# Kernel tuning notes

Measured on AMD Instinct MI355X. Metric: run time of the kernel, lower is better.

## Reference

```python
import jax, jax.numpy as jnp
import numpy as np

N = 8192       # nodes per graph
E = 262144     # edges per graph (avg degree 32)
D_IN, D_H, D_OUT = 128, 256, 64


def _gcn_layer(x, src, dst, W, b, n):
    # PyG GCNConv: add self-loops, symmetric normalization D^-1/2 (A+I) D^-1/2, then + bias
    xw = x @ W
    loop = jnp.arange(n)
    src_f = jnp.concatenate([src, loop])
    dst_f = jnp.concatenate([dst, loop])
    deg = jax.ops.segment_sum(jnp.ones(src_f.shape[0], x.dtype), dst_f, num_segments=n)
    dinv = jax.lax.rsqrt(jnp.maximum(deg, jnp.asarray(1e-12, x.dtype)))
    norm = dinv[src_f] * dinv[dst_f]                      # [E+N]
    msg = xw[src_f] * norm[:, None]                       # gather + scale
    return jax.ops.segment_sum(msg, dst_f, num_segments=n) + b


def _cross_attn(x1, x2, q, k, v):
    Q = x1 @ q
    V = x1 @ v
    K = x2 @ k
    e = jax.nn.leaky_relu(Q @ K.T, negative_slope=0.01)  # [N1, N2]
    attn = jax.nn.softmax(e, axis=-1)
    return attn @ V


def setup_inputs() -> dict:
    key = jax.random.key(0)
    ks = jax.random.split(key, 20)
    std = 1.0 / np.sqrt(D_OUT)

    def gw(k, shape, fan_in):
        return jax.random.normal(k, shape, jnp.float32) * (1.0 / np.sqrt(fan_in))

    def uw(k, shape):
        return jax.random.uniform(k, shape, jnp.float32, -std, std)

    inp = {
        'graph_set1': jax.random.randint(ks[0], (2, E), 0, N),
        'graph_set2': jax.random.randint(ks[1], (2, E), 0, N),
        'x_set1': jax.random.normal(ks[2], (N, D_IN), jnp.float32),
        'x_set2': jax.random.normal(ks[3], (N, D_IN), jnp.float32),
        'W11': gw(ks[4], (D_IN, D_H), D_IN),  'b11': jnp.zeros((D_H,), jnp.float32),
        'W12': gw(ks[5], (D_H, D_OUT), D_H),  'b12': jnp.zeros((D_OUT,), jnp.float32),
        'W21': gw(ks[6], (D_IN, D_H), D_IN),  'b21': jnp.zeros((D_H,), jnp.float32),
        'W22': gw(ks[7], (D_H, D_OUT), D_H),  'b22': jnp.zeros((D_OUT,), jnp.float32),
        'q1': uw(ks[8], (D_OUT, D_OUT)), 'k1': uw(ks[9], (D_OUT, D_OUT)), 'v1': uw(ks[10], (D_OUT, D_OUT)),
        'q2': uw(ks[11], (D_OUT, D_OUT)), 'k2': uw(ks[12], (D_OUT, D_OUT)), 'v2': uw(ks[13], (D_OUT, D_OUT)),
    }
    return inp


def reference(graph_set1, graph_set2, x_set1, x_set2,
              W11, b11, W12, b12, W21, b21, W22, b22,
              q1, k1, v1, q2, k2, v2):
    s1, d1 = graph_set1[0], graph_set1[1]
    s2, d2 = graph_set2[0], graph_set2[1]
    # GCN branch 1
    h1 = jax.nn.relu(_gcn_layer(x_set1, s1, d1, W11, b11, N))
    h1 = _gcn_layer(h1, s1, d1, W12, b12, N)
    # GCN branch 2
    h2 = jax.nn.relu(_gcn_layer(x_set2, s2, d2, W21, b21, N))
    h2 = _gcn_layer(h2, s2, d2, W22, b22, N)
    # cross attention fusion (note cross2 consumes the updated out_set1)
    o1 = _cross_attn(h1, h2, q1, k1, v1)
    o2 = _cross_attn(h2, o1, q2, k2, v2)
    logits = (o1 @ o2.T).ravel()                          # [N*N]
    return logits
```

## Files before the change

### kernel.cpp

```cpp
#include <hip/hip_runtime.h>
#include <math.h>

static constexpr int NN = 8192;
static constexpr int NE = 262144;
static constexpr int NCH = 8;
static constexpr int NS = (NN / NCH) / 32;

typedef short bfrag __attribute__((ext_vector_type(8)));
typedef float f32x4 __attribute__((ext_vector_type(4)));

#define MFMA(a, b, c) __builtin_amdgcn_mfma_f32_16x16x32_bf16((a), (b), (c), 0, 0, 0)
#define CVTPK(d, a, b) \
  asm("v_cvt_pk_bf16_f32 %0, %1, %2" : "=v"(d) : "v"(a), "v"(b))

__device__ __forceinline__ unsigned short f2bf(float x) {
  union { float f; unsigned u; } v; v.f = x;
  unsigned r = v.u + 0x7fffu + ((v.u >> 16) & 1u);
  return (unsigned short)(r >> 16);
}
__device__ __forceinline__ float bf2f(unsigned short h) {
  union { unsigned u; float f; } v; v.u = ((unsigned)h) << 16;
  return v.f;
}

__device__ __forceinline__ void gll16(const void* g, void* l) {
  __builtin_amdgcn_global_load_lds(
      (const __attribute__((address_space(1))) unsigned*)g,
      (__attribute__((address_space(3))) unsigned*)l, 16, 0, 0);
}


__global__ void k_count2(const int* __restrict__ d1, const int* __restrict__ d2,
                         int* __restrict__ i1, int* __restrict__ i2) {
  int t = blockIdx.x * 256 + threadIdx.x;
  const int* d = blockIdx.y ? d2 : d1;
  int* ii = blockIdx.y ? i2 : i1;
  if (t < NE) atomicAdd(&ii[d[t]], 1);
}

__global__ void k_scan2(const int* __restrict__ ideg1, int* __restrict__ off1,
                        int* __restrict__ cur1, float* __restrict__ dinv1,
                        const int* __restrict__ ideg2, int* __restrict__ off2,
                        int* __restrict__ cur2, float* __restrict__ dinv2) {
  const int* indeg = blockIdx.x ? ideg2 : ideg1;
  int* off = blockIdx.x ? off2 : off1;
  int* cur = blockIdx.x ? cur2 : cur1;
  float* dinv = blockIdx.x ? dinv2 : dinv1;
  __shared__ int wsum[16];
  int t = threadIdx.x, lane = t & 63, wv = t >> 6;
  int carry = 0;
  for (int base = 0; base < NN; base += 1024) {
    int v = indeg[base + t];
    int sc = v;
#pragma unroll
    for (int d = 1; d < 64; d <<= 1) {
      int o = __shfl_up(sc, d);
      if (lane >= d) sc += o;
    }
    if (lane == 63) wsum[wv] = sc;
    __syncthreads();
    if (t < 16) {
      int w = wsum[t];
#pragma unroll
      for (int d = 1; d < 16; d <<= 1) {
        int o = __shfl_up(w, d);
        if (t >= d) w += o;
      }
      wsum[t] = w;
    }
    __syncthreads();
    int excl = carry + (wv ? wsum[wv - 1] : 0) + sc - v;
    off[base + t] = excl;
    cur[base + t] = excl;
    dinv[base + t] = 1.0f / sqrtf((float)(v + 1));
    carry += wsum[15];
    __syncthreads();
  }
  if (t == 0) off[NN] = carry;
}

__global__ void k_fill2(const int* __restrict__ s1, const int* __restrict__ d1,
                        int* __restrict__ c1, int* __restrict__ l1,
                        const int* __restrict__ s2, const int* __restrict__ d2,
                        int* __restrict__ c2, int* __restrict__ l2) {
  int t = blockIdx.x * 256 + threadIdx.x;
  const int* src = blockIdx.y ? s2 : s1;
  const int* dst = blockIdx.y ? d2 : d1;
  int* cur = blockIdx.y ? c2 : c1;
  int* out = blockIdx.y ? l2 : l1;
  if (t < NE) {
    int d = dst[t];
    int slot = atomicAdd(&cur[d], 1);
    out[slot] = src[t];
  }
}


__global__ void k_split_w(const float* W11, const float* W21, const float* W12,
                          const float* W22, const float* q1, const float* k1,
                          const float* v1, const float* q2, const float* k2,
                          const float* v2, short* __restrict__ whi,
                          short* __restrict__ wlo) {
  int y = blockIdx.y;
  const float* src; int R, C, base;
  if (y == 0)      { src = W11; R = 128; C = 256; base = 0; }
  else if (y == 1) { src = W21; R = 128; C = 256; base = 32768; }
  else if (y == 2) { src = W12; R = 256; C = 64;  base = 65536; }
  else if (y == 3) { src = W22; R = 256; C = 64;  base = 81920; }
  else if (y == 4) { src = q1;  R = 64;  C = 64;  base = 98304; }
  else if (y == 5) { src = k1;  R = 64;  C = 64;  base = 102400; }
  else if (y == 6) { src = v1;  R = 64;  C = 64;  base = 106496; }
  else if (y == 7) { src = q2;  R = 64;  C = 64;  base = 110592; }
  else if (y == 8) { src = k2;  R = 64;  C = 64;  base = 114688; }
  else             { src = v2;  R = 64;  C = 64;  base = 118784; }
  int idx = blockIdx.x * 256 + threadIdx.x;
  if (idx >= R * C) return;
  int r = idx / C, c = idx % C;
  float x = src[idx];
  unsigned short h = f2bf(x);
  whi[base + c * R + r] = (short)h;
  wlo[base + c * R + r] = (short)f2bf(x - bf2f(h));
}


__global__ __launch_bounds__(256) void k_agg1d(
    const float* __restrict__ x1, const float* __restrict__ x2,
    const int* __restrict__ off1, const int* __restrict__ srcl1,
    const float* __restrict__ dinv1, const int* __restrict__ off2,
    const int* __restrict__ srcl2, const float* __restrict__ dinv2,
    short* __restrict__ a1hi, short* __restrict__ a1lo,
    short* __restrict__ a2hi, short* __restrict__ a2lo) {
  int br = blockIdx.y;
  const float* x = br ? x2 : x1;
  const int* off = br ? off2 : off1;
  const int* srcl = br ? srcl2 : srcl1;
  const float* dinv = br ? dinv2 : dinv1;
  short* ahi = br ? a2hi : a1hi;
  short* alo = br ? a2lo : a1lo;
  int wave = threadIdx.x >> 6, lane = threadIdx.x & 63;
  int node = blockIdx.x * 4 + wave;
  float dn = dinv[node];
  const float2* xr = (const float2*)x;
  float ax, ay;
  { float2 v = xr[(size_t)node * 64 + lane]; ax = dn * v.x; ay = dn * v.y; }
  int p = off[node], e = off[node + 1];
  for (; p + 3 < e; p += 4) {
    int s0 = srcl[p], s1 = srcl[p + 1], s2 = srcl[p + 2], s3 = srcl[p + 3];
    float w0 = dinv[s0], w1 = dinv[s1], w2 = dinv[s2], w3 = dinv[s3];
    float2 v0 = xr[(size_t)s0 * 64 + lane], v1 = xr[(size_t)s1 * 64 + lane];
    float2 v2 = xr[(size_t)s2 * 64 + lane], v3 = xr[(size_t)s3 * 64 + lane];
    ax += w0 * v0.x + w1 * v1.x + w2 * v2.x + w3 * v3.x;
    ay += w0 * v0.y + w1 * v1.y + w2 * v2.y + w3 * v3.y;
  }
  for (; p < e; ++p) {
    int s = srcl[p];
    float w = dinv[s];
    float2 v = xr[(size_t)s * 64 + lane];
    ax += w * v.x; ay += w * v.y;
  }
  float ox = dn * ax, oy = dn * ay;
  unsigned short hx = f2bf(ox), hy = f2bf(oy);
  int o = node * 128 + lane * 2;
  *(short2*)(ahi + o) = make_short2((short)hx, (short)hy);
  *(short2*)(alo + o) = make_short2((short)f2bf(ox - bf2f(hx)),
                                    (short)f2bf(oy - bf2f(hy)));
}


__global__ __launch_bounds__(256) void k_agg2d(
    const float* __restrict__ t1, const float* __restrict__ t2,
    const int* __restrict__ off1, const int* __restrict__ srcl1,
    const float* __restrict__ dinv1, const int* __restrict__ off2,
    const int* __restrict__ srcl2, const float* __restrict__ dinv2,
    const float* __restrict__ b12, const float* __restrict__ b22,
    short* __restrict__ g1hi, short* __restrict__ g1lo,
    short* __restrict__ g2hi, short* __restrict__ g2lo) {
  int br = blockIdx.y;
  const float* t = br ? t2 : t1;
  const int* off = br ? off2 : off1;
  const int* srcl = br ? srcl2 : srcl1;
  const float* dinv = br ? dinv2 : dinv1;
  const float* bias = br ? b22 : b12;
  short* ghi = br ? g2hi : g1hi;
  short* glo = br ? g2lo : g1lo;
  int wave = threadIdx.x >> 6, lane = threadIdx.x & 63;
  int node = blockIdx.x * 4 + wave;
  float dn = dinv[node];
  float acc = dn * t[(size_t)node * 64 + lane];
  int p = off[node], e = off[node + 1];
  for (; p + 3 < e; p += 4) {
    int s0 = srcl[p], s1 = srcl[p + 1], s2 = srcl[p + 2], s3 = srcl[p + 3];
    float w0 = dinv[s0], w1 = dinv[s1], w2 = dinv[s2], w3 = dinv[s3];
    acc += w0 * t[(size_t)s0 * 64 + lane] + w1 * t[(size_t)s1 * 64 + lane] +
           w2 * t[(size_t)s2 * 64 + lane] + w3 * t[(size_t)s3 * 64 + lane];
  }
  for (; p < e; ++p) {
    int s = srcl[p];
    acc += dinv[s] * t[(size_t)s * 64 + lane];
  }
  float o = dn * acc + bias[lane];
  unsigned short h = f2bf(o);
  ghi[(size_t)node * 64 + lane] = (short)h;
  glo[(size_t)node * 64 + lane] = (short)f2bf(o - bf2f(h));
}


__global__ __launch_bounds__(64) void k_gemmL1(
    const short* __restrict__ a1hi, const short* __restrict__ a1lo,
    const short* __restrict__ a2hi, const short* __restrict__ a2lo,
    const short* __restrict__ whi, const short* __restrict__ wlo,
    const float* __restrict__ b11, const float* __restrict__ b21,
    short* __restrict__ h1hi, short* __restrict__ h1lo,
    short* __restrict__ h2hi, short* __restrict__ h2lo) {
  int br = blockIdx.z;
  const short* Ahi = br ? a2hi : a1hi;
  const short* Alo = br ? a2lo : a1lo;
  const short* Bh = whi + (br ? 32768 : 0);
  const short* Bl = wlo + (br ? 32768 : 0);
  const float* bias = br ? b21 : b11;
  short* Chi = br ? h2hi : h1hi;
  short* Clo = br ? h2lo : h1lo;
  int lane = threadIdx.x;
  int lo16 = lane & 15, hi4 = lane >> 4;
  int r0 = blockIdx.x * 16;
  int c0 = blockIdx.y * 64;
  bfrag ah[4], al[4];
  const char* abh = (const char*)Ahi + ((size_t)(r0 + lo16) * 128 + hi4 * 8) * 2;
  const char* abl = (const char*)Alo + ((size_t)(r0 + lo16) * 128 + hi4 * 8) * 2;
#pragma unroll
  for (int ks = 0; ks < 4; ++ks) {
    ah[ks] = *(const bfrag*)(abh + ks * 64);
    al[ks] = *(const bfrag*)(abl + ks * 64);
  }
  f32x4 z = {0.f, 0.f, 0.f, 0.f};
  f32x4 acc[4] = {z, z, z, z};
#pragma unroll
  for (int c = 0; c < 4; ++c) {
    const char* bbh = (const char*)Bh + ((size_t)(c0 + c * 16 + lo16) * 128 + hi4 * 8) * 2;
    const char* bbl = (const char*)Bl + ((size_t)(c0 + c * 16 + lo16) * 128 + hi4 * 8) * 2;
#pragma unroll
    for (int ks = 0; ks < 4; ++ks) {
      bfrag bh = *(const bfrag*)(bbh + ks * 64);
      bfrag bl = *(const bfrag*)(bbl + ks * 64);
      acc[c] = MFMA(ah[ks], bh, acc[c]);
      acc[c] = MFMA(ah[ks], bl, acc[c]);
      acc[c] = MFMA(al[ks], bh, acc[c]);
    }
  }
#pragma unroll
  for (int c = 0; c < 4; ++c) {
    int col = c0 + c * 16 + lo16;
    float bv = bias[col];
#pragma unroll
    for (int r = 0; r < 4; ++r) {
      int row = r0 + hi4 * 4 + r;
      float v = fmaxf(acc[c][r] + bv, 0.f);
      unsigned short h = f2bf(v);
      Chi[(size_t)row * 256 + col] = (short)h;
      Clo[(size_t)row * 256 + col] = (short)f2bf(v - bf2f(h));
    }
  }
}


__global__ __launch_bounds__(64) void k_gemmL2(
    const short* __restrict__ h1hi, const short* __restrict__ h1lo,
    const short* __restrict__ h2hi, const short* __restrict__ h2lo,
    const short* __restrict__ whi, const short* __restrict__ wlo,
    float* __restrict__ t1, float* __restrict__ t2) {
  int br = blockIdx.y;
  const short* Ahi = br ? h2hi : h1hi;
  const short* Alo = br ? h2lo : h1lo;
  const short* Bh = whi + (br ? 81920 : 65536);
  const short* Bl = wlo + (br ? 81920 : 65536);
  float* Cf = br ? t2 : t1;
  int lane = threadIdx.x;
  int lo16 = lane & 15, hi4 = lane >> 4;
  int r0 = blockIdx.x * 16;
  bfrag ah[8], al[8];
  const char* abh = (const char*)Ahi + ((size_t)(r0 + lo16) * 256 + hi4 * 8) * 2;
  const char* abl = (const char*)Alo + ((size_t)(r0 + lo16) * 256 + hi4 * 8) * 2;
#pragma unroll
  for (int ks = 0; ks < 8; ++ks) {
    ah[ks] = *(const bfrag*)(abh + ks * 64);
    al[ks] = *(const bfrag*)(abl + ks * 64);
  }
  f32x4 z = {0.f, 0.f, 0.f, 0.f};
  f32x4 acc[4] = {z, z, z, z};
#pragma unroll
  for (int c = 0; c < 4; ++c) {
    const char* bbh = (const char*)Bh + ((size_t)(c * 16 + lo16) * 256 + hi4 * 8) * 2;
    const char* bbl = (const char*)Bl + ((size_t)(c * 16 + lo16) * 256 + hi4 * 8) * 2;
#pragma unroll
    for (int ks = 0; ks < 8; ++ks) {
      bfrag bh = *(const bfrag*)(bbh + ks * 64);
      bfrag bl = *(const bfrag*)(bbl + ks * 64);
      acc[c] = MFMA(ah[ks], bh, acc[c]);
      acc[c] = MFMA(ah[ks], bl, acc[c]);
      acc[c] = MFMA(al[ks], bh, acc[c]);
    }
  }
#pragma unroll
  for (int c = 0; c < 4; ++c) {
    int col = c * 16 + lo16;
#pragma unroll
    for (int r = 0; r < 4; ++r)
      Cf[(size_t)(r0 + hi4 * 4 + r) * 64 + col] = acc[c][r];
  }
}


__global__ __launch_bounds__(64) void k_qkv(
    const short* __restrict__ Aqhi, const short* __restrict__ Aqlo,
    const short* __restrict__ Akhi, const short* __restrict__ Aklo,
    const short* __restrict__ Avhi, const short* __restrict__ Avlo,
    const short* __restrict__ whi, const short* __restrict__ wlo,
    int bq, int bk, int bv,
    short* __restrict__ Qhi, short* __restrict__ Qlo,
    short* __restrict__ Khi, short* __restrict__ Klo,
    short* __restrict__ Vthi, short* __restrict__ Vtlo) {
  int y = blockIdx.y;
  const short *Ah, *Al;
  int boff;
  if (y == 0)      { Ah = Aqhi; Al = Aqlo; boff = bq; }
  else if (y == 1) { Ah = Akhi; Al = Aklo; boff = bk; }
  else             { Ah = Avhi; Al = Avlo; boff = bv; }
  const short* Bh = whi + boff;
  const short* Bl = wlo + boff;
  int lane = threadIdx.x;
  int lo16 = lane & 15, hi4 = lane >> 4;
  int r0 = blockIdx.x * 16;
  bfrag ah0, ah1, al0, al1;
  {
    const char* a = (const char*)(Ah + (size_t)(r0 + lo16) * 64 + hi4 * 8);
    const char* b = (const char*)(Al + (size_t)(r0 + lo16) * 64 + hi4 * 8);
    ah0 = *(const bfrag*)a; ah1 = *(const bfrag*)(a + 64);
    al0 = *(const bfrag*)b; al1 = *(const bfrag*)(b + 64);
  }
  f32x4 z = {0.f, 0.f, 0.f, 0.f};
  f32x4 acc[4] = {z, z, z, z};
#pragma unroll
  for (int c = 0; c < 4; ++c) {
    const char* bbh = (const char*)(Bh + (size_t)(c * 16 + lo16) * 64 + hi4 * 8);
    const char* bbl = (const char*)(Bl + (size_t)(c * 16 + lo16) * 64 + hi4 * 8);
    bfrag bh0 = *(const bfrag*)bbh, bh1 = *(const bfrag*)(bbh + 64);
    bfrag bl0 = *(const bfrag*)bbl, bl1 = *(const bfrag*)(bbl + 64);
    acc[c] = MFMA(ah0, bh0, acc[c]);
    acc[c] = MFMA(ah1, bh1, acc[c]);
    acc[c] = MFMA(ah0, bl0, acc[c]);
    acc[c] = MFMA(ah1, bl1, acc[c]);
    acc[c] = MFMA(al0, bh0, acc[c]);
    acc[c] = MFMA(al1, bh1, acc[c]);
  }
  if (y == 2) {
#pragma unroll
    for (int c = 0; c < 4; ++c) {
      int col = c * 16 + lo16;
      short4 vh, vl;
      float v0 = acc[c][0], v1 = acc[c][1], v2 = acc[c][2], v3 = acc[c][3];
      unsigned short h0 = f2bf(v0), h1 = f2bf(v1), h2 = f2bf(v2), h3 = f2bf(v3);
      vh = make_short4((short)h0, (short)h1, (short)h2, (short)h3);
      vl = make_short4((short)f2bf(v0 - bf2f(h0)), (short)f2bf(v1 - bf2f(h1)),
                       (short)f2bf(v2 - bf2f(h2)), (short)f2bf(v3 - bf2f(h3)));
      size_t o = (size_t)col * NN + r0 + hi4 * 4;
      *(short4*)(Vthi + o) = vh;
      *(short4*)(Vtlo + o) = vl;
    }
  } else {
    short* oh = (y == 0) ? Qhi : Khi;
    short* ol = (y == 0) ? Qlo : Klo;
#pragma unroll
    for (int c = 0; c < 4; ++c) {
      int col = c * 16 + lo16;
#pragma unroll
      for (int r = 0; r < 4; ++r) {
        int row = r0 + hi4 * 4 + r;
        float v = acc[c][r];
        unsigned short h = f2bf(v);
        oh[(size_t)row * 64 + col] = (short)h;
        ol[(size_t)row * 64 + col] = (short)f2bf(v - bf2f(h));
      }
    }
  }
}


__global__ __launch_bounds__(256) void k_attn_v8(
    const short* __restrict__ Qhi, const short* __restrict__ Qlo,
    const short* __restrict__ Khi_g, const short* __restrict__ Klo_g,
    const short* __restrict__ Vthi_g, const short* __restrict__ Vtlo_g,
    float* __restrict__ Opart, float* __restrict__ mpart, float* __restrict__ lpart) {
  __shared__ short skh[2][32 * 64], skl[2][32 * 64];
  __shared__ short svh[2][64 * 32], svl[2][64 * 32];
  __shared__ short plds[8][16 * 40];
  const int tid = threadIdx.x;
  const int wave = tid >> 6, lane = tid & 63;
  const int lo16 = lane & 15, hi4 = lane >> 4;
  const int q0 = blockIdx.x * 128 + wave * 32;
  const int j0 = blockIdx.y * (NN / NCH);
  short* mypA = plds[wave * 2];
  short* mypB = plds[wave * 2 + 1];

  const int krow = wave * 8 + (lane >> 3);
  const int kcbs = ((lane & 7) * 16) ^ ((krow & 7) << 4);
  const int vrow = wave * 16 + (lane >> 2);
  const int vcbs = ((lane & 3) * 16) ^ (((vrow >> 1) & 3) << 4);
  const char* gka = (const char*)Khi_g + (size_t)(j0 + krow) * 128 + kcbs;
  const char* gkb = (const char*)Klo_g + (size_t)(j0 + krow) * 128 + kcbs;
  const char* gva = (const char*)Vthi_g + (size_t)vrow * (NN * 2) + (size_t)j0 * 2 + vcbs;
  const char* gvb = (const char*)Vtlo_g + (size_t)vrow * (NN * 2) + (size_t)j0 * 2 + vcbs;

#define STAGE(buf, s)                                                \
  do {                                                               \
    gll16(gka + (size_t)(s) * 4096, (char*)skh[buf] + wave * 1024);  \
    gll16(gkb + (size_t)(s) * 4096, (char*)skl[buf] + wave * 1024);  \
    gll16(gva + (s) * 64, (char*)svh[buf] + wave * 1024);            \
    gll16(gvb + (s) * 64, (char*)svl[buf] + wave * 1024);            \
  } while (0)

  const bfrag* qphA = (const bfrag*)(Qhi + (size_t)(q0 + lo16) * 64 + hi4 * 8);
  const bfrag* qplA = (const bfrag*)(Qlo + (size_t)(q0 + lo16) * 64 + hi4 * 8);
  const bfrag* qphB = (const bfrag*)(Qhi + (size_t)(q0 + 16 + lo16) * 64 + hi4 * 8);
  const bfrag* qplB = (const bfrag*)(Qlo + (size_t)(q0 + 16 + lo16) * 64 + hi4 * 8);
  bfrag qh0A = qphA[0], qh1A = qphA[4], ql0A = qplA[0], ql1A = qplA[4];
  bfrag qh0B = qphB[0], qh1B = qphB[4], ql0B = qplB[0], ql1B = qplB[4];

  bfrag onesf;
#pragma unroll
  for (int i = 0; i < 8; ++i) onesf[i] = (short)0x3F80;

  f32x4 z = {0.f, 0.f, 0.f, 0.f};
  f32x4 oaccA[4] = {z, z, z, z}, oaccB[4] = {z, z, z, z};
  f32x4 oextA = z, oextB = z;
  float mrunA[4] = {-1e30f, -1e30f, -1e30f, -1e30f};
  float mrunB[4] = {-1e30f, -1e30f, -1e30f, -1e30f};

#define SMAX(sa, mrun, oacc, oext, myp, pa)                                   \
  do {                                                                        \
    _Pragma("unroll") for (int t = 0; t < 2; ++t)                             \
      _Pragma("unroll") for (int r = 0; r < 4; ++r) {                         \
        float v = sa[t][r];                                                   \
        sa[t][r] = fmaxf(v, 0.01f * v);                                       \
      }                                                                       \
    float pm[4];                                                              \
    _Pragma("unroll") for (int r = 0; r < 4; ++r)                             \
        pm[r] = fmaxf(sa[0][r], sa[1][r]);                                    \
    bool rb = false;                                                          \
    _Pragma("unroll") for (int r = 0; r < 4; ++r) rb |= (pm[r] > mrun[r] + 4.f); \
    if (__any(rb)) {   \
      _Pragma("unroll") for (int mask = 1; mask <= 8; mask <<= 1)             \
        _Pragma("unroll") for (int r = 0; r < 4; ++r)                         \
          pm[r] = fmaxf(pm[r], __shfl_xor(pm[r], mask));                      \
      _Pragma("unroll") for (int r = 0; r < 4; ++r) {                         \
        float nm = (pm[r] > mrun[r] + 4.f) ? pm[r] : mrun[r];                 \
        float c_ = __expf(mrun[r] - nm);                                      \
        _Pragma("unroll") for (int c = 0; c < 4; ++c) oacc[c][r] *= c_;       \
        oext[r] *= c_;                                                        \
        mrun[r] = nm;                                                         \
      }                                                                       \
    }                                                                         \
    float p0[4], p1[4];                                                       \
    _Pragma("unroll") for (int r = 0; r < 4; ++r) {                           \
      p0[r] = __expf(sa[0][r] - mrun[r]);                                     \
      p1[r] = __expf(sa[1][r] - mrun[r]);                                     \
    }                                                                         \
    unsigned pq0, pq1, pq2, pq3;                                              \
    CVTPK(pq0, p0[0], p0[1]);                                                 \
    CVTPK(pq1, p0[2], p0[3]);                                                 \
    CVTPK(pq2, p1[0], p1[1]);                                                 \
    CVTPK(pq3, p1[2], p1[3]);                                                 \
    {                                                                         \
      int rb_ = hi4 * 4;                                                      \
      myp[(rb_ + 0) * 40 + lo16] = (short)pq0;                                \
      myp[(rb_ + 1) * 40 + lo16] = (short)(pq0 >> 16);                        \
      myp[(rb_ + 2) * 40 + lo16] = (short)pq1;                                \
      myp[(rb_ + 3) * 40 + lo16] = (short)(pq1 >> 16);                        \
      myp[(rb_ + 0) * 40 + 16 + lo16] = (short)pq2;                           \
      myp[(rb_ + 1) * 40 + 16 + lo16] = (short)(pq2 >> 16);                   \
      myp[(rb_ + 2) * 40 + 16 + lo16] = (short)pq3;                           \
      myp[(rb_ + 3) * 40 + 16 + lo16] = (short)(pq3 >> 16);                   \
    }                                                                         \
    pa = *(const bfrag*)(myp + lo16 * 40 + hi4 * 8);                          \
  } while (0)

  auto step = [&](int buf) {
    const char* kh = (const char*)skh[buf];
    const char* kl = (const char*)skl[buf];
    f32x4 saA[2], saB[2];
    __builtin_amdgcn_s_setprio(1);
#pragma unroll
    for (int t = 0; t < 2; ++t) {
      int jr = 16 * t + lo16;
      int sw = (jr & 7) << 4;
      const char* rowh = kh + jr * 128;
      const char* rowl = kl + jr * 128;
      bfrag kf0 = *(const bfrag*)(rowh + ((hi4 * 16) ^ sw));
      bfrag kf1 = *(const bfrag*)(rowh + ((64 + hi4 * 16) ^ sw));
      bfrag kg0 = *(const bfrag*)(rowl + ((hi4 * 16) ^ sw));
      bfrag kg1 = *(const bfrag*)(rowl + ((64 + hi4 * 16) ^ sw));
      f32x4 a = z;
      a = MFMA(qh0A, kf0, a);
      a = MFMA(qh1A, kf1, a);
      a = MFMA(qh0A, kg0, a);
      a = MFMA(qh1A, kg1, a);
      a = MFMA(ql0A, kf0, a);
      a = MFMA(ql1A, kf1, a);
      saA[t] = a;
      f32x4 b = z;
      b = MFMA(qh0B, kf0, b);
      b = MFMA(qh1B, kf1, b);
      b = MFMA(qh0B, kg0, b);
      b = MFMA(qh1B, kg1, b);
      b = MFMA(ql0B, kf0, b);
      b = MFMA(ql1B, kf1, b);
      saB[t] = b;
    }
    __builtin_amdgcn_s_setprio(0);
    bfrag paA, paB;
    SMAX(saA, mrunA, oaccA, oextA, mypA, paA);
    SMAX(saB, mrunB, oaccB, oextB, mypB, paB);
    const char* vh = (const char*)svh[buf];
    const char* vl = (const char*)svl[buf];
    __builtin_amdgcn_s_setprio(1);
#pragma unroll
    for (int c = 0; c < 4; ++c) {
      int dv = 16 * c + lo16;
      int svw = ((dv >> 1) & 3) << 4;
      bfrag vhf = *(const bfrag*)(vh + dv * 64 + ((hi4 * 16) ^ svw));
      bfrag vlf = *(const bfrag*)(vl + dv * 64 + ((hi4 * 16) ^ svw));
      oaccA[c] = MFMA(paA, vhf, oaccA[c]);
      oaccA[c] = MFMA(paA, vlf, oaccA[c]);
      oaccB[c] = MFMA(paB, vhf, oaccB[c]);
      oaccB[c] = MFMA(paB, vlf, oaccB[c]);
    }
    oextA = MFMA(paA, onesf, oextA);
    oextB = MFMA(paB, onesf, oextB);
    __builtin_amdgcn_s_setprio(0);
  };

  STAGE(0, 0);
  STAGE(1, 1);
  for (int s = 0; s < NS - 1; ++s) {
    const int buf = s & 1;
    asm volatile("s_waitcnt vmcnt(4)" ::: "memory");
    __builtin_amdgcn_s_barrier();
    __builtin_amdgcn_sched_barrier(0);
    step(buf);
    __builtin_amdgcn_sched_barrier(0);
    __builtin_amdgcn_s_barrier();
    if (s + 2 < NS) STAGE(buf, s + 2);
  }
  asm volatile("s_waitcnt vmcnt(0)" ::: "memory");
  __builtin_amdgcn_s_barrier();
  __builtin_amdgcn_sched_barrier(0);
  step((NS - 1) & 1);
#undef STAGE
#undef SMAX

#pragma unroll
  for (int c = 0; c < 4; ++c)
#pragma unroll
    for (int r = 0; r < 4; ++r) {
      Opart[((size_t)blockIdx.y * NN + q0 + hi4 * 4 + r) * 64 + 16 * c + lo16] = oaccA[c][r];
      Opart[((size_t)blockIdx.y * NN + q0 + 16 + hi4 * 4 + r) * 64 + 16 * c + lo16] = oaccB[c][r];
    }
  if (lo16 == 0) {
#pragma unroll
    for (int r = 0; r < 4; ++r) {
      mpart[blockIdx.y * NN + q0 + hi4 * 4 + r] = mrunA[r];
      lpart[blockIdx.y * NN + q0 + hi4 * 4 + r] = oextA[r];
      mpart[blockIdx.y * NN + q0 + 16 + hi4 * 4 + r] = mrunB[r];
      lpart[blockIdx.y * NN + q0 + 16 + hi4 * 4 + r] = oextB[r];
    }
  }
}

__global__ void k_comb(const float* __restrict__ Opart,
                       const float* __restrict__ mpart,
                       const float* __restrict__ lpart,
                       short* __restrict__ Ohi, short* __restrict__ Olo) {
  int row = blockIdx.x * 4 + (threadIdx.x >> 6);
  int d = threadIdx.x & 63;
  float M = -1e30f;
  for (int i = 0; i < NCH; ++i) M = fmaxf(M, mpart[i * NN + row]);
  float L = 0.f, acc = 0.f;
  for (int i = 0; i < NCH; ++i) {
    float w = __expf(mpart[i * NN + row] - M);
    L += w * lpart[i * NN + row];
    acc += w * Opart[((size_t)i * NN + row) * 64 + d];
  }
  float o = acc / L;
  unsigned short h = f2bf(o);
  Ohi[(size_t)row * 64 + d] = (short)h;
  Olo[(size_t)row * 64 + d] = (short)f2bf(o - bf2f(h));
}


__global__ __launch_bounds__(256) void k_outer(const short* __restrict__ o1hi,
                                               const short* __restrict__ o1lo,
                                               const short* __restrict__ o2hi,
                                               const short* __restrict__ o2lo,
                                               float* __restrict__ out) {
  int wave = threadIdx.x >> 6, lane = threadIdx.x & 63;
  int lo16 = lane & 15, hi4 = lane >> 4;
  int i0 = blockIdx.x * 128 + wave * 32;
  const bfrag* aphA = (const bfrag*)(o1hi + (size_t)(i0 + lo16) * 64 + hi4 * 8);
  const bfrag* aplA = (const bfrag*)(o1lo + (size_t)(i0 + lo16) * 64 + hi4 * 8);
  const bfrag* aphB = (const bfrag*)(o1hi + (size_t)(i0 + 16 + lo16) * 64 + hi4 * 8);
  const bfrag* aplB = (const bfrag*)(o1lo + (size_t)(i0 + 16 + lo16) * 64 + hi4 * 8);
  bfrag ah0A = aphA[0], ah1A = aphA[4], al0A = aplA[0], al1A = aplA[4];
  bfrag ah0B = aphB[0], ah1B = aphB[4], al0B = aplB[0], al1B = aplB[4];
  f32x4 z = {0.f, 0.f, 0.f, 0.f};
  int jbase = blockIdx.y * (NN / 16);

#define LOADB(JV, BH0, BH1, BL0, BL1)                                        \
  do {                                                                       \
    const bfrag* bph = (const bfrag*)(o2hi + (size_t)((JV) + lo16) * 64 + hi4 * 8); \
    const bfrag* bpl = (const bfrag*)(o2lo + (size_t)((JV) + lo16) * 64 + hi4 * 8); \
    BH0 = bph[0]; BH1 = bph[4]; BL0 = bpl[0]; BL1 = bpl[4];                  \
  } while (0)

#define COMP(JV, BH0, BH1, BL0, BL1)                                  \
  do {                                                                \
    f32x4 accA = z, accB = z;                                         \
    accA = MFMA(ah0A, BH0, accA);                                     \
    accA = MFMA(ah1A, BH1, accA);                                     \
    accA = MFMA(ah0A, BL0, accA);                                     \
    accA = MFMA(ah1A, BL1, accA);                                     \
    accA = MFMA(al0A, BH0, accA);                                     \
    accA = MFMA(al1A, BH1, accA);                                     \
    accB = MFMA(ah0B, BH0, accB);                                     \
    accB = MFMA(ah1B, BH1, accB);                                     \
    accB = MFMA(ah0B, BL0, accB);                                     \
    accB = MFMA(ah1B, BL1, accB);                                     \
    accB = MFMA(al0B, BH0, accB);                                     \
    accB = MFMA(al1B, BH1, accB);                                     \
    _Pragma("unroll")                                                 \
    for (int r = 0; r < 4; ++r) {                                     \
      out[(size_t)(i0 + hi4 * 4 + r) * NN + (JV) + lo16] = accA[r];   \
      out[(size_t)(i0 + 16 + hi4 * 4 + r) * NN + (JV) + lo16] = accB[r]; \
    }                                                                 \
  } while (0)

  bfrag pah0, pah1, pal0, pal1, pbh0, pbh1, pbl0, pbl1;
  LOADB(jbase, pah0, pah1, pal0, pal1);
  for (int jt = 0; jt < NN / 16 / 16; jt += 2) {
    int ja = jbase + jt * 16;
    LOADB(ja + 16, pbh0, pbh1, pbl0, pbl1);
    COMP(ja, pah0, pah1, pal0, pal1);
    if (jt + 2 < NN / 16 / 16) LOADB(ja + 32, pah0, pah1, pal0, pal1);
    COMP(ja + 16, pbh0, pbh1, pbl0, pbl1);
  }
#undef LOADB
#undef COMP
}


extern "C" void kernel_launch(void* const* d_in, const int* in_sizes, int n_in,
                              void* d_out, int out_size, void* d_ws, size_t ws_size,
                              hipStream_t stream) {
  const int* g1 = (const int*)d_in[0];
  const int* g2 = (const int*)d_in[1];
  const float* x1 = (const float*)d_in[2];
  const float* x2 = (const float*)d_in[3];
  const float* W11 = (const float*)d_in[4];
  const float* b11 = (const float*)d_in[5];
  const float* W12 = (const float*)d_in[6];
  const float* b12 = (const float*)d_in[7];
  const float* W21 = (const float*)d_in[8];
  const float* b21 = (const float*)d_in[9];
  const float* W22 = (const float*)d_in[10];
  const float* b22 = (const float*)d_in[11];
  const float* q1 = (const float*)d_in[12];
  const float* k1 = (const float*)d_in[13];
  const float* v1 = (const float*)d_in[14];
  const float* q2 = (const float*)d_in[15];
  const float* k2 = (const float*)d_in[16];
  const float* v2 = (const float*)d_in[17];

  char* ob = (char*)d_out;
  const size_t MB = 1u << 20;
  int* srcl1 = (int*)(ob + 0 * MB);
  int* srcl2 = (int*)(ob + 1 * MB);
  char* small = ob + 2 * MB;
  int* ideg1 = (int*)(small);
  int* ideg2 = (int*)(small + (32u << 10));
  int* off1 = (int*)(small + (64u << 10));
  int* off2 = (int*)(small + (128u << 10));
  int* cur1 = (int*)(small + (192u << 10));
  int* cur2 = (int*)(small + (256u << 10));
  float* dinv1 = (float*)(small + (320u << 10));
  float* dinv2 = (float*)(small + (384u << 10));
  short* whi = (short*)(ob + 3 * MB);
  short* wlo = (short*)(ob + 3 * MB + (512u << 10));
  short* a1hi = (short*)(ob + 4 * MB);
  short* a1lo = (short*)(ob + 6 * MB);
  short* a2hi = (short*)(ob + 8 * MB);
  short* a2lo = (short*)(ob + 10 * MB);
  short* h1hi = (short*)(ob + 12 * MB);
  short* h1lo = (short*)(ob + 16 * MB);
  short* h2hi = (short*)(ob + 20 * MB);
  short* h2lo = (short*)(ob + 24 * MB);
  float* tbuf1 = (float*)(ob + 28 * MB);
  float* tbuf2 = (float*)(ob + 30 * MB);
  short* g1hi = (short*)(ob + 32 * MB);
  short* g1lo = (short*)(ob + 33 * MB);
  short* g2hi = (short*)(ob + 34 * MB);
  short* g2lo = (short*)(ob + 35 * MB);
  short* Qhi = (short*)(ob + 36 * MB);
  short* Qlo = (short*)(ob + 37 * MB);
  short* Khi = (short*)(ob + 38 * MB);
  short* Klo = (short*)(ob + 39 * MB);
  short* Vthi = (short*)(ob + 40 * MB);
  short* Vtlo = (short*)(ob + 41 * MB);
  float* Opart = (float*)(ob + 42 * MB);
  float* mpart = (float*)(ob + 58 * MB);
  float* lpart = (float*)(ob + 58 * MB + (256u << 10));
  short* o1hi = (short*)d_ws;
  short* o1lo = (short*)((char*)d_ws + 1 * MB);
  short* o2hi = (short*)((char*)d_ws + 2 * MB);
  short* o2lo = (short*)((char*)d_ws + 3 * MB);

  hipMemsetAsync(ideg1, 0, 64u << 10, stream);
  k_count2<<<dim3(1024, 2), 256, 0, stream>>>(g1 + NE, g2 + NE, ideg1, ideg2);
  k_scan2<<<2, 1024, 0, stream>>>(ideg1, off1, cur1, dinv1, ideg2, off2, cur2, dinv2);
  k_fill2<<<dim3(1024, 2), 256, 0, stream>>>(g1, g1 + NE, cur1, srcl1,
                                             g2, g2 + NE, cur2, srcl2);
  k_split_w<<<dim3(128, 10), 256, 0, stream>>>(W11, W21, W12, W22, q1, k1, v1,
                                               q2, k2, v2, whi, wlo);

  k_agg1d<<<dim3(2048, 2), 256, 0, stream>>>(x1, x2, off1, srcl1, dinv1,
                                             off2, srcl2, dinv2,
                                             a1hi, a1lo, a2hi, a2lo);
  k_gemmL1<<<dim3(512, 4, 2), 64, 0, stream>>>(a1hi, a1lo, a2hi, a2lo, whi, wlo,
                                               b11, b21, h1hi, h1lo, h2hi, h2lo);
  k_gemmL2<<<dim3(512, 2), 64, 0, stream>>>(h1hi, h1lo, h2hi, h2lo, whi, wlo,
                                            tbuf1, tbuf2);
  k_agg2d<<<dim3(2048, 2), 256, 0, stream>>>(tbuf1, tbuf2, off1, srcl1, dinv1,
                                             off2, srcl2, dinv2, b12, b22,
                                             g1hi, g1lo, g2hi, g2lo);

  k_qkv<<<dim3(512, 3), 64, 0, stream>>>(g1hi, g1lo, g2hi, g2lo, g1hi, g1lo,
                                         whi, wlo, 98304, 102400, 106496,
                                         Qhi, Qlo, Khi, Klo, Vthi, Vtlo);
  k_attn_v8<<<dim3(64, NCH), 256, 0, stream>>>(Qhi, Qlo, Khi, Klo, Vthi, Vtlo,
                                               Opart, mpart, lpart);
  k_comb<<<2048, 256, 0, stream>>>(Opart, mpart, lpart, o1hi, o1lo);

  k_qkv<<<dim3(512, 3), 64, 0, stream>>>(g2hi, g2lo, o1hi, o1lo, g2hi, g2lo,
                                         whi, wlo, 110592, 114688, 118784,
                                         Qhi, Qlo, Khi, Klo, Vthi, Vtlo);
  k_attn_v8<<<dim3(64, NCH), 256, 0, stream>>>(Qhi, Qlo, Khi, Klo, Vthi, Vtlo,
                                               Opart, mpart, lpart);
  k_comb<<<2048, 256, 0, stream>>>(Opart, mpart, lpart, o2hi, o2lo);

  k_outer<<<dim3(64, 16), 256, 0, stream>>>(o1hi, o1lo, o2hi, o2lo, (float*)d_out);

  (void)in_sizes; (void)n_in; (void)out_size; (void)ws_size;
}
```

Before: 636.2 us.

## Replace LDS-staged attention with single-wave direct-load kernel and exp2 softmax

The attention kernel no longer uses four-wave blocks that stage K and V tiles into shared memory with double-buffered async loads and barriers. It becomes a one-wave-per-block kernel that reads K and V fragments directly from global memory, relying on cache. Separately, the Q weights are prescaled by log2(e) so the softmax and combine steps can use exp2f instead of __expf. This drops barriers and LDS traffic and gives more, smaller blocks, but loses cross-wave reuse of K/V tiles and the explicit load/compute overlap.

Result: slower. 767.8 us (+20.7%).

```diff
diff --git a/kernel.cpp b/kernel.cpp
--- a/kernel.cpp
+++ b/kernel.cpp
@@ -5,6 +5,7 @@
 static constexpr int NE = 262144;
 static constexpr int NCH = 8;
 static constexpr int NS = (NN / NCH) / 32;
+static constexpr float L2E = 1.44269504088896340736f;
 
 typedef short bfrag __attribute__((ext_vector_type(8)));
 typedef float f32x4 __attribute__((ext_vector_type(4)));
@@ -21,12 +22,6 @@
 __device__ __forceinline__ float bf2f(unsigned short h) {
   union { unsigned u; float f; } v; v.u = ((unsigned)h) << 16;
   return v.f;
-}
-
-__device__ __forceinline__ void gll16(const void* g, void* l) {
-  __builtin_amdgcn_global_load_lds(
-      (const __attribute__((address_space(1))) unsigned*)g,
-      (__attribute__((address_space(3))) unsigned*)l, 16, 0, 0);
 }
 
 
@@ -102,21 +97,21 @@
                           const float* v2, short* __restrict__ whi,
                           short* __restrict__ wlo) {
   int y = blockIdx.y;
-  const float* src; int R, C, base;
+  const float* src; int R, C, base; float sc = 1.f;
   if (y == 0)      { src = W11; R = 128; C = 256; base = 0; }
   else if (y == 1) { src = W21; R = 128; C = 256; base = 32768; }
   else if (y == 2) { src = W12; R = 256; C = 64;  base = 65536; }
   else if (y == 3) { src = W22; R = 256; C = 64;  base = 81920; }
-  else if (y == 4) { src = q1;  R = 64;  C = 64;  base = 98304; }
+  else if (y == 4) { src = q1;  R = 64;  C = 64;  base = 98304; sc = L2E; }
   else if (y == 5) { src = k1;  R = 64;  C = 64;  base = 102400; }
   else if (y == 6) { src = v1;  R = 64;  C = 64;  base = 106496; }
-  else if (y == 7) { src = q2;  R = 64;  C = 64;  base = 110592; }
+  else if (y == 7) { src = q2;  R = 64;  C = 64;  base = 110592; sc = L2E; }
   else if (y == 8) { src = k2;  R = 64;  C = 64;  base = 114688; }
   else             { src = v2;  R = 64;  C = 64;  base = 118784; }
   int idx = blockIdx.x * 256 + threadIdx.x;
   if (idx >= R * C) return;
   int r = idx / C, c = idx % C;
-  float x = src[idx];
+  float x = src[idx] * sc;
   unsigned short h = f2bf(x);
   whi[base + c * R + r] = (short)h;
   wlo[base + c * R + r] = (short)f2bf(x - bf2f(h));
@@ -385,38 +380,18 @@
 }
 
 
-__global__ __launch_bounds__(256) void k_attn_v8(
+__global__ __launch_bounds__(64) void k_attn_v9(
     const short* __restrict__ Qhi, const short* __restrict__ Qlo,
     const short* __restrict__ Khi_g, const short* __restrict__ Klo_g,
     const short* __restrict__ Vthi_g, const short* __restrict__ Vtlo_g,
     float* __restrict__ Opart, float* __restrict__ mpart, float* __restrict__ lpart) {
-  __shared__ short skh[2][32 * 64], skl[2][32 * 64];
-  __shared__ short svh[2][64 * 32], svl[2][64 * 32];
-  __shared__ short plds[8][16 * 40];
-  const int tid = threadIdx.x;
-  const int wave = tid >> 6, lane = tid & 63;
+  __shared__ short plds[2][16 * 40];
+  const int lane = threadIdx.x;
   const int lo16 = lane & 15, hi4 = lane >> 4;
-  const int q0 = blockIdx.x * 128 + wave * 32;
+  const int q0 = blockIdx.x * 32;
   const int j0 = blockIdx.y * (NN / NCH);
-  short* mypA = plds[wave * 2];
-  short* mypB = plds[wave * 2 + 1];
-
-  const int krow = wave * 8 + (lane >> 3);
-  const int kcbs = ((lane & 7) * 16) ^ ((krow & 7) << 4);
-  const int vrow = wave * 16 + (lane >> 2);
-  const int vcbs = ((lane & 3) * 16) ^ (((vrow >> 1) & 3) << 4);
-  const char* gka = (const char*)Khi_g + (size_t)(j0 + krow) * 128 + kcbs;
-  const char* gkb = (const char*)Klo_g + (size_t)(j0 + krow) * 128 + kcbs;
-  const char* gva = (const char*)Vthi_g + (size_t)vrow * (NN * 2) + (size_t)j0 * 2 + vcbs;
-  const char* gvb = (const char*)Vtlo_g + (size_t)vrow * (NN * 2) + (size_t)j0 * 2 + vcbs;
-
-#define STAGE(buf, s)                                                \
-  do {                                                               \
-    gll16(gka + (size_t)(s) * 4096, (char*)skh[buf] + wave * 1024);  \
-    gll16(gkb + (size_t)(s) * 4096, (char*)skl[buf] + wave * 1024);  \
-    gll16(gva + (s) * 64, (char*)svh[buf] + wave * 1024);            \
-    gll16(gvb + (s) * 64, (char*)svl[buf] + wave * 1024);            \
-  } while (0)
+  short* mypA = plds[0];
+  short* mypB = plds[1];
 
   const bfrag* qphA = (const bfrag*)(Qhi + (size_t)(q0 + lo16) * 64 + hi4 * 8);
   const bfrag* qplA = (const bfrag*)(Qlo + (size_t)(q0 + lo16) * 64 + hi4 * 8);
@@ -434,6 +409,7 @@
   f32x4 oextA = z, oextB = z;
   float mrunA[4] = {-1e30f, -1e30f, -1e30f, -1e30f};
   float mrunB[4] = {-1e30f, -1e30f, -1e30f, -1e30f};
+  const float THR = 4.f * L2E;
 
 #define SMAX(sa, mrun, oacc, oext, myp, pa)                                   \
   do {                                                                        \
@@ -446,14 +422,14 @@
     _Pragma("unroll") for (int r = 0; r < 4; ++r)                             \
         pm[r] = fmaxf(sa[0][r], sa[1][r]);                                    \
     bool rb = false;                                                          \
-    _Pragma("unroll") for (int r = 0; r < 4; ++r) rb |= (pm[r] > mrun[r] + 4.f); \
-    if (__any(rb)) {   \
+    _Pragma("unroll") for (int r = 0; r < 4; ++r) rb |= (pm[r] > mrun[r] + THR); \
+    if (__any(rb)) {                         \
       _Pragma("unroll") for (int mask = 1; mask <= 8; mask <<= 1)             \
         _Pragma("unroll") for (int r = 0; r < 4; ++r)                         \
           pm[r] = fmaxf(pm[r], __shfl_xor(pm[r], mask));                      \
       _Pragma("unroll") for (int r = 0; r < 4; ++r) {                         \
-        float nm = (pm[r] > mrun[r] + 4.f) ? pm[r] : mrun[r];                 \
-        float c_ = __expf(mrun[r] - nm);                                      \
+        float nm = (pm[r] > mrun[r] + THR) ? pm[r] : mrun[r];                 \
+        float c_ = exp2f(mrun[r] - nm);                                       \
         _Pragma("unroll") for (int c = 0; c < 4; ++c) oacc[c][r] *= c_;       \
         oext[r] *= c_;                                                        \
         mrun[r] = nm;                                                         \
@@ -461,8 +437,8 @@
     }                                                                         \
     float p0[4], p1[4];                                                       \
     _Pragma("unroll") for (int r = 0; r < 4; ++r) {                           \
-      p0[r] = __expf(sa[0][r] - mrun[r]);                                     \
-      p1[r] = __expf(sa[1][r] - mrun[r]);                                     \
+      p0[r] = exp2f(sa[0][r] - mrun[r]);                                      \
+      p1[r] = exp2f(sa[1][r] - mrun[r]);                                      \
     }                                                                         \
     unsigned pq0, pq1, pq2, pq3;                                              \
     CVTPK(pq0, p0[0], p0[1]);                                                 \
@@ -483,21 +459,18 @@
     pa = *(const bfrag*)(myp + lo16 * 40 + hi4 * 8);                          \
   } while (0)
 
-  auto step = [&](int buf) {
-    const char* kh = (const char*)skh[buf];
-    const char* kl = (const char*)skl[buf];
+  for (int s = 0; s < NS; ++s) {
+    const int jb = j0 + s * 32;
     f32x4 saA[2], saB[2];
     __builtin_amdgcn_s_setprio(1);
 #pragma unroll
     for (int t = 0; t < 2; ++t) {
-      int jr = 16 * t + lo16;
-      int sw = (jr & 7) << 4;
-      const char* rowh = kh + jr * 128;
-      const char* rowl = kl + jr * 128;
-      bfrag kf0 = *(const bfrag*)(rowh + ((hi4 * 16) ^ sw));
-      bfrag kf1 = *(const bfrag*)(rowh + ((64 + hi4 * 16) ^ sw));
-      bfrag kg0 = *(const bfrag*)(rowl + ((hi4 * 16) ^ sw));
-      bfrag kg1 = *(const bfrag*)(rowl + ((64 + hi4 * 16) ^ sw));
+      const char* rowh = (const char*)(Khi_g + (size_t)(jb + 16 * t + lo16) * 64 + hi4 * 8);
+      const char* rowl = (const char*)(Klo_g + (size_t)(jb + 16 * t + lo16) * 64 + hi4 * 8);
+      bfrag kf0 = *(const bfrag*)(rowh);
+      bfrag kf1 = *(const bfrag*)(rowh + 64);
+      bfrag kg0 = *(const bfrag*)(rowl);
+      bfrag kg1 = *(const bfrag*)(rowl + 64);
       f32x4 a = z;
       a = MFMA(qh0A, kf0, a);
       a = MFMA(qh1A, kf1, a);
@@ -516,45 +489,27 @@
       saB[t] = b;
     }
     __builtin_amdgcn_s_setprio(0);
+    bfrag vhf[4], vlf[4];
+#pragma unroll
+    for (int c = 0; c < 4; ++c) {
+      vhf[c] = *(const bfrag*)(Vthi_g + (size_t)(16 * c + lo16) * NN + jb + hi4 * 8);
+      vlf[c] = *(const bfrag*)(Vtlo_g + (size_t)(16 * c + lo16) * NN + jb + hi4 * 8);
+    }
     bfrag paA, paB;
     SMAX(saA, mrunA, oaccA, oextA, mypA, paA);
     SMAX(saB, mrunB, oaccB, oextB, mypB, paB);
-    const char* vh = (const char*)svh[buf];
-    const char* vl = (const char*)svl[buf];
     __builtin_amdgcn_s_setprio(1);
 #pragma unroll
     for (int c = 0; c < 4; ++c) {
-      int dv = 16 * c + lo16;
-      int svw = ((dv >> 1) & 3) << 4;
-      bfrag vhf = *(const bfrag*)(vh + dv * 64 + ((hi4 * 16) ^ svw));
-      bfrag vlf = *(const bfrag*)(vl + dv * 64 + ((hi4 * 16) ^ svw));
-      oaccA[c] = MFMA(paA, vhf, oaccA[c]);
-      oaccA[c] = MFMA(paA, vlf, oaccA[c]);
-      oaccB[c] = MFMA(paB, vhf, oaccB[c]);
-      oaccB[c] = MFMA(paB, vlf, oaccB[c]);
+      oaccA[c] = MFMA(paA, vhf[c], oaccA[c]);
+      oaccA[c] = MFMA(paA, vlf[c], oaccA[c]);
+      oaccB[c] = MFMA(paB, vhf[c], oaccB[c]);
+      oaccB[c] = MFMA(paB, vlf[c], oaccB[c]);
     }
     oextA = MFMA(paA, onesf, oextA);
     oextB = MFMA(paB, onesf, oextB);
     __builtin_amdgcn_s_setprio(0);
-  };
-
-  STAGE(0, 0);
-  STAGE(1, 1);
-  for (int s = 0; s < NS - 1; ++s) {
-    const int buf = s & 1;
-    asm volatile("s_waitcnt vmcnt(4)" ::: "memory");
-    __builtin_amdgcn_s_barrier();
-    __builtin_amdgcn_sched_barrier(0);
-    step(buf);
-    __builtin_amdgcn_sched_barrier(0);
-    __builtin_amdgcn_s_barrier();
-    if (s + 2 < NS) STAGE(buf, s + 2);
-  }
-  asm volatile("s_waitcnt vmcnt(0)" ::: "memory");
-  __builtin_amdgcn_s_barrier();
-  __builtin_amdgcn_sched_barrier(0);
-  step((NS - 1) & 1);
-#undef STAGE
+  }
 #undef SMAX
 
 #pragma unroll
@@ -585,7 +540,7 @@
   for (int i = 0; i < NCH; ++i) M = fmaxf(M, mpart[i * NN + row]);
   float L = 0.f, acc = 0.f;
   for (int i = 0; i < NCH; ++i) {
-    float w = __expf(mpart[i * NN + row] - M);
+    float w = exp2f(mpart[i * NN + row] - M);
     L += w * lpart[i * NN + row];
     acc += w * Opart[((size_t)i * NN + row) * 64 + d];
   }
@@ -743,14 +698,14 @@
   k_qkv<<<dim3(512, 3), 64, 0, stream>>>(g1hi, g1lo, g2hi, g2lo, g1hi, g1lo,
                                          whi, wlo, 98304, 102400, 106496,
                                          Qhi, Qlo, Khi, Klo, Vthi, Vtlo);
-  k_attn_v8<<<dim3(64, NCH), 256, 0, stream>>>(Qhi, Qlo, Khi, Klo, Vthi, Vtlo,
+  k_attn_v9<<<dim3(256, NCH), 64, 0, stream>>>(Qhi, Qlo, Khi, Klo, Vthi, Vtlo,
                                                Opart, mpart, lpart);
   k_comb<<<2048, 256, 0, stream>>>(Opart, mpart, lpart, o1hi, o1lo);
 
   k_qkv<<<dim3(512, 3), 64, 0, stream>>>(g2hi, g2lo, o1hi, o1lo, g2hi, g2lo,
                                          whi, wlo, 110592, 114688, 118784,
                                          Qhi, Qlo, Khi, Klo, Vthi, Vtlo);
-  k_attn_v8<<<dim3(64, NCH), 256, 0, stream>>>(Qhi, Qlo, Khi, Klo, Vthi, Vtlo,
+  k_attn_v9<<<dim3(256, NCH), 64, 0, stream>>>(Qhi, Qlo, Khi, Klo, Vthi, Vtlo,
                                                Opart, mpart, lpart);
   k_comb<<<2048, 256, 0, stream>>>(Opart, mpart, lpart, o2hi, o2lo);
 
```
